# Kernel optimization log

Hardware: AMD Instinct MI355X
Metric: run time of the kernel (lower is better)

## Reference

```python
import math
import jax, jax.numpy as jnp
import numpy as np


def setup_inputs() -> dict:
    key = jax.random.key(0)
    ks = jax.random.split(key, 6)
    b, k, t, h = 4, 128, 2048, 8
    s = 0.05
    return {
        "x": jax.random.normal(ks[0], (b, k, t), dtype=jnp.float32),
        "Wq": jax.random.normal(ks[1], (h * k, k), dtype=jnp.float32) * s,
        "Wk": jax.random.normal(ks[2], (h * k, k), dtype=jnp.float32) * s,
        "Wv": jax.random.normal(ks[3], (h * k, k), dtype=jnp.float32) * s,
        "Wu": jax.random.normal(ks[4], (k, h * k), dtype=jnp.float32) * s,
        "bu": jax.random.normal(ks[5], (k,), dtype=jnp.float32) * s,
    }


def reference(x, Wq, Wk, Wv, Wu, bu):
    b, k, t = x.shape
    h = Wq.shape[0] // k

    def proj(W):
        # x: [b,k,t], W: [h*k, k] -> [b,h,k,t]
        return jnp.einsum('bkt,jk->bjt', x, W).reshape(b, h, k, t)

    q = proj(Wq)
    keys = proj(Wk)
    v = proj(Wv)

    # scores: [b,h,t,t], scaled by 1/sqrt(k)
    dot = jnp.einsum('bhkt,bhki->bhti', q, keys) / math.sqrt(k)
    attn = jax.nn.softmax(dot, axis=-1)

    # attend: [b,h,k,t]
    o = jnp.einsum('bhti,bhki->bhkt', attn, v)

    # unify heads: Wu [k, h*k] viewed as [k,h,k]
    Wu3 = Wu.reshape(k, h, k)
    out = jnp.einsum('bhet,khe->bkt', o, Wu3)
    return out + bu[None, :, None]
```

## Files before the change

kernel.cpp:

```cpp
#include <hip/hip_runtime.h>
#include <hip/hip_bf16.h>

using short8 = __attribute__((ext_vector_type(8))) short;
using f32x4  = __attribute__((ext_vector_type(4))) float;
using f32x16 = __attribute__((ext_vector_type(16))) float;
using uint2v = __attribute__((ext_vector_type(2))) unsigned;

#define B_  4
#define KD  128
#define T_  2048
#define H_  8
#define HK  (H_*KD)
#define NT  (T_/64)
#define VROW 72

__device__ __forceinline__ ushort f2bf(float f) {
    unsigned u = __builtin_bit_cast(unsigned, f);
    u += 0x7fffu + ((u >> 16) & 1u);
    return (ushort)(u >> 16);
}

__device__ __forceinline__ unsigned cvt_pk_bf16(float lo, float hi) {
    unsigned r;
    asm("v_cvt_pk_bf16_f32 %0, %1, %2" : "=v"(r) : "v"(lo), "v"(hi));
    return r;
}

__device__ __forceinline__ unsigned cvt_pk_fp8_lo(unsigned old, float a, float b) {
    unsigned r = old;
    asm("v_cvt_pk_fp8_f32 %0, %1, %2" : "+v"(r) : "v"(a), "v"(b));
    return r;
}
__device__ __forceinline__ unsigned cvt_pk_fp8_hi(unsigned old, float a, float b) {
    unsigned r = old;
    asm("v_cvt_pk_fp8_f32 %0, %1, %2 op_sel:[0,0,1]" : "+v"(r) : "v"(a), "v"(b));
    return r;
}

__global__ __launch_bounds__(256) void prep_kernel(const float* __restrict__ x,
                                                   const float* __restrict__ Wq,
                                                   const float* __restrict__ Wk,
                                                   const float* __restrict__ Wv,
                                                   const float* __restrict__ Wu,
                                                   ushort* __restrict__ wdst,
                                                   ushort* __restrict__ xt) {
    __shared__ float tile[64][65];
    int bx = blockIdx.x;
    if (bx < 2048) {
        int i = bx * 256 + threadIdx.x;
        const int n1 = HK * KD;
        const float* src = (i < n1) ? Wq : (i < 2*n1) ? Wk : (i < 3*n1) ? Wv : Wu;
        wdst[i] = f2bf(src[i & (n1 - 1)]);
        return;
    }
    int bi = bx - 2048;
    int t0 = (bi & 31) * 64;
    int k0 = ((bi >> 5) & 1) * 64;
    int b  = bi >> 6;
    int c  = threadIdx.x & 63;
    int r4 = threadIdx.x >> 6;
    #pragma unroll
    for (int i = 0; i < 16; i++) {
        int k = r4 * 16 + i;
        tile[k][c] = x[((size_t)b * KD + k0 + k) * T_ + t0 + c];
    }
    __syncthreads();
    #pragma unroll
    for (int i = 0; i < 16; i++) {
        int t = r4 * 16 + i;
        xt[((size_t)b * T_ + t0 + t) * KD + k0 + c] = f2bf(tile[c][t]);
    }
}

__global__ __launch_bounds__(256, 2) void proj_kernel(const ushort* __restrict__ xt,
                                                      const ushort* __restrict__ wall,
                                                      ushort* __restrict__ qtb,
                                                      ushort* __restrict__ ktb,
                                                      unsigned char* __restrict__ vsb) {
    int bz = blockIdx.y;
    int which = bz >> 2, b = bz & 3;
    int tidb = blockIdx.x;
    const ushort *A, *Bp;
    void* Cv;
    int N, m0, n0;
    float scale = 1.f;
    if (which < 2) {
        m0 = (tidb >> 3) * 128;
        n0 = (tidb & 7) * 128;
        A  = xt + (size_t)b * T_ * KD;
        Bp = wall + (size_t)which * (HK * KD);
        Cv = (which ? ktb : qtb) + (size_t)b * T_ * HK;
        N  = HK;
        if (which == 0) scale = 0.08838834764831845f;
    } else {
        m0 = (tidb >> 4) * 128;
        n0 = (tidb & 15) * 128;
        A  = wall + (size_t)2 * (HK * KD);
        Bp = xt + (size_t)b * T_ * KD;
        Cv = vsb + (size_t)b * HK * T_;
        N  = T_;
    }
    int lane = threadIdx.x & 63;
    int w    = threadIdx.x >> 6;
    int lq = lane & 31, hi = lane >> 5, hi8 = hi * 8;
    m0 += (w >> 1) * 64;
    n0 += (w & 1) * 64;

    const ushort* a0p = A  + (size_t)(m0 + lq) * KD + hi8;
    const ushort* a1p = A  + (size_t)(m0 + 32 + lq) * KD + hi8;
    const ushort* b0p = Bp + (size_t)(n0 + lq) * KD + hi8;
    const ushort* b1p = Bp + (size_t)(n0 + 32 + lq) * KD + hi8;

    short8 a0[8], a1[8], b0[8], b1[8];
    #pragma unroll
    for (int kc = 0; kc < 8; kc++) {
        a0[kc] = *(const short8*)(a0p + kc * 16);
        a1[kc] = *(const short8*)(a1p + kc * 16);
        b0[kc] = *(const short8*)(b0p + kc * 16);
        b1[kc] = *(const short8*)(b1p + kc * 16);
    }
    f32x16 acc[2][2] = {};
    #pragma unroll
    for (int kc = 0; kc < 8; kc++) {
        acc[0][0] = __builtin_amdgcn_mfma_f32_32x32x16_bf16(a0[kc], b0[kc], acc[0][0], 0, 0, 0);
        acc[0][1] = __builtin_amdgcn_mfma_f32_32x32x16_bf16(a0[kc], b1[kc], acc[0][1], 0, 0, 0);
        acc[1][0] = __builtin_amdgcn_mfma_f32_32x32x16_bf16(a1[kc], b0[kc], acc[1][0], 0, 0, 0);
        acc[1][1] = __builtin_amdgcn_mfma_f32_32x32x16_bf16(a1[kc], b1[kc], acc[1][1], 0, 0, 0);
    }
    if (which < 2) {
        ushort* C = (ushort*)Cv;
        #pragma unroll
        for (int i = 0; i < 2; i++)
            #pragma unroll
            for (int j = 0; j < 2; j++)
                #pragma unroll
                for (int r = 0; r < 16; r++) {
                    int m = m0 + i*32 + (r & 3) + 8 * (r >> 2) + 4 * hi;
                    int n = n0 + j*32 + lq;
                    C[(size_t)m * N + n] = f2bf(acc[i][j][r] * scale);
                }
    } else {
        unsigned char* C = (unsigned char*)Cv;
        #pragma unroll
        for (int i = 0; i < 2; i++)
            #pragma unroll
            for (int j = 0; j < 2; j++)
                #pragma unroll
                for (int r = 0; r < 16; r++) {
                    int m = m0 + i*32 + (r & 3) + 8 * (r >> 2) + 4 * hi;
                    int n = n0 + j*32 + lq;
                    float v = acc[i][j][r];
                    C[(size_t)m * N + n] = (unsigned char)(cvt_pk_fp8_lo(0u, v, v) & 0xffu);
                }
    }
}

__global__ __launch_bounds__(256) void gemm_abT_f32bias(const ushort* __restrict__ A,
                                                        const ushort* __restrict__ B, long sB,
                                                        const float* __restrict__ bias,
                                                        float* __restrict__ C, long sC,
                                                        int M, int N, int Kd) {
    int b = blockIdx.z;
    B += (long)b * sB;  C += (long)b * sC;
    int lane = threadIdx.x & 63;
    int w    = threadIdx.x >> 6;
    int lr = lane & 15, lg = lane >> 4;
    int m0 = blockIdx.x * 64 + (w >> 1) * 32;
    int n0 = blockIdx.y * 64 + (w & 1) * 32;

    f32x4 acc[2][2] = {};
    #pragma unroll 4
    for (int k0 = 0; k0 < Kd; k0 += 32) {
        short8 af[2], bf[2];
        #pragma unroll
        for (int i = 0; i < 2; i++)
            af[i] = *(const short8*)(A + (long)(m0 + i*16 + lr) * Kd + k0 + lg*8);
        #pragma unroll
        for (int j = 0; j < 2; j++)
            bf[j] = *(const short8*)(B + (long)(n0 + j*16 + lr) * Kd + k0 + lg*8);
        #pragma unroll
        for (int i = 0; i < 2; i++)
            #pragma unroll
            for (int j = 0; j < 2; j++)
                acc[i][j] = __builtin_amdgcn_mfma_f32_16x16x32_bf16(af[i], bf[j], acc[i][j], 0, 0, 0);
    }
    #pragma unroll
    for (int i = 0; i < 2; i++)
        #pragma unroll
        for (int j = 0; j < 2; j++)
            #pragma unroll
            for (int r = 0; r < 4; r++) {
                int m = m0 + i*16 + lg*4 + r;
                int n = n0 + j*16 + lr;
                C[(long)m * N + n] = acc[i][j][r] + bias[m];
            }
}

__global__ __launch_bounds__(512, 2) void attn32_kernel(const ushort* __restrict__ qt,
                                                        const ushort* __restrict__ kt,
                                                        const unsigned char* __restrict__ vs,
                                                        ushort* __restrict__ ot) {
    int f = blockIdx.x;
    int xcd = f & 7, u = f >> 3;
    int qt8 = u & 7, gh = u >> 3;
    int g = xcd + 8 * gh;
    int h = g & 7, b = g >> 3;
    int w    = threadIdx.x >> 6;
    int lane = threadIdx.x & 63;
    int lq = lane & 31, hi = lane >> 5;
    int hi8 = hi * 8;
    int q0w = qt8 * 256 + w * 32;

    __shared__ __align__(16) ushort k_lds[2][64 * 128];
    __shared__ __align__(16) unsigned char v_lds[2][128 * VROW];

    int tid  = threadIdx.x;
    int krow = tid >> 3, kcol = (tid & 7) << 4;
    const ushort* kst = kt + ((size_t)b * T_ + krow) * HK + h * KD + kcol;
    int kwi = krow * 128 + (kcol ^ ((krow & 7) << 3));
    int vrow = tid >> 2, vc16 = (tid & 3) << 4;
    const unsigned char* vst = vs + ((size_t)b * HK + h * KD + vrow) * T_ + vc16;
    int vwb = vrow * VROW + ((((vc16 >> 4) ^ (vrow & 3))) << 4);

    const ushort* qbase = qt + ((size_t)b * T_ + q0w + lq) * HK + h * KD + hi8;

    short8 qf[8];
    #pragma unroll
    for (int dc = 0; dc < 8; dc++)
        qf[dc] = *(const short8*)(qbase + dc * 16);

    short8 rk0 = *(const short8*)(kst);
    short8 rk1 = *(const short8*)(kst + 8);
    long rvlo = *(const long*)(vst);
    long rvhi = *(const long*)(vst + 8);
    *(short8*)&k_lds[0][kwi]     = rk0;
    *(short8*)&k_lds[0][kwi ^ 8] = rk1;
    *(long*)&v_lds[0][vwb]       = rvlo;
    *(long*)&v_lds[0][vwb + 8]   = rvhi;
    rk0 = *(const short8*)(kst + (size_t)64 * HK);
    rk1 = *(const short8*)(kst + (size_t)64 * HK + 8);
    rvlo = *(const long*)(vst + 64);
    rvhi = *(const long*)(vst + 64 + 8);
    __syncthreads();

    f32x16 o_acc[4] = {};
    float m_q = -1e30f, l_q = 0.f;
    const int xsw = (lq & 7) << 3;
    const int vsw = lq & 3;

    for (int t = 0; t < NT; ++t) {
        const int cur = t & 1;
        f32x16 s0 = {}, s1 = {};
        const ushort* kr0 = &k_lds[cur][(size_t)lq * 128];
        const ushort* kr1 = &k_lds[cur][(size_t)(32 + lq) * 128];
        #pragma unroll
        for (int dc = 0; dc < 8; dc++) {
            int c = (dc * 16 + hi8) ^ xsw;
            short8 kf0 = *(const short8*)(kr0 + c);
            short8 kf1 = *(const short8*)(kr1 + c);
            s0 = __builtin_amdgcn_mfma_f32_32x32x16_bf16(kf0, qf[dc], s0, 0, 0, 0);
            s1 = __builtin_amdgcn_mfma_f32_32x32x16_bf16(kf1, qf[dc], s1, 0, 0, 0);
        }

        float mx[8];
        #pragma unroll
        for (int i = 0; i < 8; i++)
            mx[i] = fmaxf(fmaxf(s0[i], s0[i+8]), fmaxf(s1[i], s1[i+8]));
        #pragma unroll
        for (int st = 4; st > 0; st >>= 1)
            #pragma unroll
            for (int i = 0; i < st; i++) mx[i] = fmaxf(mx[i], mx[i+st]);
        float pmax = fmaxf(mx[0], __shfl_xor(mx[0], 32));

        if (!__all(pmax - m_q <= 5.f)) {
            float mnew = fmaxf(m_q, pmax);
            float corr = __expf(m_q - mnew);
            l_q *= corr;
            m_q = mnew;
            #pragma unroll
            for (int r = 0; r < 16; r++) {
                float cr = __shfl(corr, (r & 3) + 8 * (r >> 2) + 4 * hi);
                #pragma unroll
                for (int dn = 0; dn < 4; dn++) o_acc[dn][r] *= cr;
            }
        }

        float ls0 = 0.f, ls1 = 0.f, ls2 = 0.f, ls3 = 0.f;
        #pragma unroll
        for (int r = 0; r < 16; r++) {
            float e0 = __expf(s0[r] - m_q);
            float e1 = __expf(s1[r] - m_q);
            s0[r] = e0; s1[r] = e1;
            if (r & 1) { ls1 += e0; ls3 += e1; } else { ls0 += e0; ls2 += e1; }
        }
        float lsum = (ls0 + ls1) + (ls2 + ls3);
        lsum += __shfl_xor(lsum, 32);
        l_q += lsum;

        long ap8[4];
        #pragma unroll
        for (int ks = 0; ks < 4; ks++) {
            const f32x16& sN = (ks < 2) ? s0 : s1;
            int rb = (ks & 1) * 8;
            unsigned F0 = cvt_pk_fp8_lo(0u, sN[rb+0], sN[rb+1]);
            F0 = cvt_pk_fp8_hi(F0, sN[rb+2], sN[rb+3]);
            unsigned F1 = cvt_pk_fp8_lo(0u, sN[rb+4], sN[rb+5]);
            F1 = cvt_pk_fp8_hi(F1, sN[rb+6], sN[rb+7]);
            uint2v d01 = __builtin_amdgcn_permlane32_swap(F0, F1, false, false);
            ap8[ks] = (long)(((unsigned long)d01[1] << 32) | (unsigned long)d01[0]);
        }

        #pragma unroll
        for (int dn = 0; dn < 4; dn++) {
            const unsigned char* vr = &v_lds[cur][(size_t)(dn*32 + lq) * VROW];
            #pragma unroll
            for (int ks = 0; ks < 4; ks++) {
                long vf = *(const long*)(vr + ((ks ^ vsw) << 4) + hi8);
                o_acc[dn] = __builtin_amdgcn_mfma_f32_32x32x16_fp8_fp8(ap8[ks], vf, o_acc[dn], 0, 0, 0);
            }
        }

        __syncthreads();
        if (t + 1 < NT) {
            const int nxt = cur ^ 1;
            *(short8*)&k_lds[nxt][kwi]     = rk0;
            *(short8*)&k_lds[nxt][kwi ^ 8] = rk1;
            *(long*)&v_lds[nxt][vwb]       = rvlo;
            *(long*)&v_lds[nxt][vwb + 8]   = rvhi;
            if (t + 2 < NT) {
                size_t ko = (size_t)(t + 2) * 64 * HK;
                int    vo = (t + 2) * 64;
                rk0 = *(const short8*)(kst + ko);
                rk1 = *(const short8*)(kst + ko + 8);
                rvlo = *(const long*)(vst + vo);
                rvhi = *(const long*)(vst + vo + 8);
            }
            __syncthreads();
        }
    }

    float linv = 1.f / l_q;
    ushort* ob = ot + ((size_t)b * T_ + q0w) * HK + h * KD;
    #pragma unroll
    for (int r = 0; r < 16; r++) {
        int qrow = (r & 3) + 8 * (r >> 2) + 4 * hi;
        float lr_ = __shfl(linv, qrow);
        #pragma unroll
        for (int dn = 0; dn < 4; dn++)
            ob[(size_t)qrow * HK + dn*32 + lq] = f2bf(o_acc[dn][r] * lr_);
    }
}

extern "C" void kernel_launch(void* const* d_in, const int* in_sizes, int n_in,
                              void* d_out, int out_size, void* d_ws, size_t ws_size,
                              hipStream_t stream) {
    const float* x  = (const float*)d_in[0];
    const float* Wq = (const float*)d_in[1];
    const float* Wk = (const float*)d_in[2];
    const float* Wv = (const float*)d_in[3];
    const float* Wu = (const float*)d_in[4];
    const float* bu = (const float*)d_in[5];
    float* out = (float*)d_out;

    const size_t XT  = (size_t)B_ * T_ * KD * 2;
    const size_t WB  = (size_t)HK * KD * 2;
    const size_t BIG = (size_t)B_ * T_ * HK * 2;
    const size_t VSZ = (size_t)B_ * HK * T_;
    size_t need = XT + 4*WB + 3*BIG + VSZ;
    if (ws_size < need) return;

    char* p = (char*)d_ws;
    ushort* xt  = (ushort*)p;            p += XT;
    ushort* wqb = (ushort*)p;            p += WB;
    ushort* wkb = (ushort*)p;            p += WB;
    ushort* wvb = (ushort*)p;            p += WB;
    ushort* wub = (ushort*)p;            p += WB;
    ushort* qtb = (ushort*)p;            p += BIG;
    ushort* ktb = (ushort*)p;            p += BIG;
    unsigned char* vsb = (unsigned char*)p;  p += VSZ;
    ushort* otb = (ushort*)p;            p += BIG;
    (void)wkb; (void)wvb;

    prep_kernel<<<2304, 256, 0, stream>>>(x, Wq, Wk, Wv, Wu, wqb, xt);

    proj_kernel<<<dim3(128, 12), 256, 0, stream>>>(xt, wqb, qtb, ktb, vsb);

    attn32_kernel<<<dim3(256), 512, 0, stream>>>(qtb, ktb, vsb, otb);

    gemm_abT_f32bias<<<dim3(KD/64, T_/64, B_), 256, 0, stream>>>(
        wub, otb, (long)T_*HK, bu, out, (long)KD*T_, KD, T_, HK);
}
```

Before: 122.8 us.

## Read K directly from global in attention and vectorize projection stores

The attention kernel no longer stages K tiles through double-buffered LDS. Each wave loads its K fragments straight from global memory (L2-cached) inside the loop, which frees LDS and removes the K store/swizzle work. The cost is redundant global K reads across the 8 waves and exposed load latency with no prefetch. The projection kernel also swaps its output tiling so each lane writes packed bf16x4 or fp8x4 words instead of scalar strided stores.

```diff
diff --git a/kernel.cpp b/kernel.cpp
--- a/kernel.cpp
+++ b/kernel.cpp
@@ -18,12 +18,6 @@
     unsigned u = __builtin_bit_cast(unsigned, f);
     u += 0x7fffu + ((u >> 16) & 1u);
     return (ushort)(u >> 16);
-}
-
-__device__ __forceinline__ unsigned cvt_pk_bf16(float lo, float hi) {
-    unsigned r;
-    asm("v_cvt_pk_bf16_f32 %0, %1, %2" : "=v"(r) : "v"(lo), "v"(hi));
-    return r;
 }
 
 __device__ __forceinline__ unsigned cvt_pk_fp8_lo(unsigned old, float a, float b) {
@@ -80,36 +74,34 @@
     int bz = blockIdx.y;
     int which = bz >> 2, b = bz & 3;
     int tidb = blockIdx.x;
-    const ushort *A, *Bp;
-    void* Cv;
-    int N, m0, n0;
-    float scale = 1.f;
-    if (which < 2) {
-        m0 = (tidb >> 3) * 128;
-        n0 = (tidb & 7) * 128;
-        A  = xt + (size_t)b * T_ * KD;
-        Bp = wall + (size_t)which * (HK * KD);
-        Cv = (which ? ktb : qtb) + (size_t)b * T_ * HK;
-        N  = HK;
-        if (which == 0) scale = 0.08838834764831845f;
-    } else {
-        m0 = (tidb >> 4) * 128;
-        n0 = (tidb & 15) * 128;
-        A  = wall + (size_t)2 * (HK * KD);
-        Bp = xt + (size_t)b * T_ * KD;
-        Cv = vsb + (size_t)b * HK * T_;
-        N  = T_;
-    }
     int lane = threadIdx.x & 63;
     int w    = threadIdx.x >> 6;
     int lq = lane & 31, hi = lane >> 5, hi8 = hi * 8;
-    m0 += (w >> 1) * 64;
-    n0 += (w & 1) * 64;
-
-    const ushort* a0p = A  + (size_t)(m0 + lq) * KD + hi8;
-    const ushort* a1p = A  + (size_t)(m0 + 32 + lq) * KD + hi8;
-    const ushort* b0p = Bp + (size_t)(n0 + lq) * KD + hi8;
-    const ushort* b1p = Bp + (size_t)(n0 + 32 + lq) * KD + hi8;
+
+    int tt0 = (tidb >> 3) * 128;
+    int jj0 = (tidb & 7) * 128;
+
+    const ushort *a0p, *a1p, *b0p, *b1p;
+    int m0, n0;
+    if (which < 2) {
+        m0 = jj0 + (w >> 1) * 64;
+        n0 = tt0 + (w & 1) * 64;
+        const ushort* A  = wall + (size_t)which * (HK * KD);
+        const ushort* Bp = xt + (size_t)b * T_ * KD;
+        a0p = A  + (size_t)(m0 + lq) * KD + hi8;
+        a1p = A  + (size_t)(m0 + 32 + lq) * KD + hi8;
+        b0p = Bp + (size_t)(n0 + lq) * KD + hi8;
+        b1p = Bp + (size_t)(n0 + 32 + lq) * KD + hi8;
+    } else {
+        m0 = tt0 + (w >> 1) * 64;
+        n0 = jj0 + (w & 1) * 64;
+        const ushort* A  = xt + (size_t)b * T_ * KD;
+        const ushort* Bp = wall + (size_t)2 * (HK * KD);
+        a0p = A  + (size_t)(m0 + lq) * KD + hi8;
+        a1p = A  + (size_t)(m0 + 32 + lq) * KD + hi8;
+        b0p = Bp + (size_t)(n0 + lq) * KD + hi8;
+        b1p = Bp + (size_t)(n0 + 32 + lq) * KD + hi8;
+    }
 
     short8 a0[8], a1[8], b0[8], b1[8];
     #pragma unroll
@@ -127,31 +119,43 @@
         acc[1][0] = __builtin_amdgcn_mfma_f32_32x32x16_bf16(a1[kc], b0[kc], acc[1][0], 0, 0, 0);
         acc[1][1] = __builtin_amdgcn_mfma_f32_32x32x16_bf16(a1[kc], b1[kc], acc[1][1], 0, 0, 0);
     }
+
     if (which < 2) {
-        ushort* C = (ushort*)Cv;
+        float scale = which ? 1.f : 0.08838834764831845f;
+        ushort* C = (which ? ktb : qtb) + (size_t)b * T_ * HK;
         #pragma unroll
         for (int i = 0; i < 2; i++)
             #pragma unroll
-            for (int j = 0; j < 2; j++)
+            for (int jj = 0; jj < 2; jj++) {
+                int t = n0 + jj*32 + lq;
                 #pragma unroll
-                for (int r = 0; r < 16; r++) {
-                    int m = m0 + i*32 + (r & 3) + 8 * (r >> 2) + 4 * hi;
-                    int n = n0 + j*32 + lq;
-                    C[(size_t)m * N + n] = f2bf(acc[i][j][r] * scale);
+                for (int qd = 0; qd < 4; qd++) {
+                    int jb = m0 + i*32 + 8*qd + 4*hi;
+                    const f32x16& a = acc[i][jj];
+                    unsigned u0 = (unsigned)f2bf(a[4*qd+0]*scale)
+                                | ((unsigned)f2bf(a[4*qd+1]*scale) << 16);
+                    unsigned u1 = (unsigned)f2bf(a[4*qd+2]*scale)
+                                | ((unsigned)f2bf(a[4*qd+3]*scale) << 16);
+                    uint2v uv; uv[0] = u0; uv[1] = u1;
+                    *(uint2v*)(C + (size_t)t * HK + jb) = uv;
                 }
+            }
     } else {
-        unsigned char* C = (unsigned char*)Cv;
+        unsigned char* C = vsb + (size_t)b * HK * T_;
         #pragma unroll
         for (int i = 0; i < 2; i++)
             #pragma unroll
-            for (int j = 0; j < 2; j++)
+            for (int jj = 0; jj < 2; jj++) {
+                int j = n0 + jj*32 + lq;
                 #pragma unroll
-                for (int r = 0; r < 16; r++) {
-                    int m = m0 + i*32 + (r & 3) + 8 * (r >> 2) + 4 * hi;
-                    int n = n0 + j*32 + lq;
-                    float v = acc[i][j][r];
-                    C[(size_t)m * N + n] = (unsigned char)(cvt_pk_fp8_lo(0u, v, v) & 0xffu);
+                for (int qd = 0; qd < 4; qd++) {
+                    int tb = m0 + i*32 + 8*qd + 4*hi;
+                    const f32x16& a = acc[i][jj];
+                    unsigned dw = cvt_pk_fp8_lo(0u, a[4*qd+0], a[4*qd+1]);
+                    dw = cvt_pk_fp8_hi(dw, a[4*qd+2], a[4*qd+3]);
+                    *(unsigned*)(C + (size_t)j * T_ + tb) = dw;
                 }
+            }
     }
 }
 
@@ -211,53 +215,43 @@
     int hi8 = hi * 8;
     int q0w = qt8 * 256 + w * 32;
 
-    __shared__ __align__(16) ushort k_lds[2][64 * 128];
     __shared__ __align__(16) unsigned char v_lds[2][128 * VROW];
 
     int tid  = threadIdx.x;
-    int krow = tid >> 3, kcol = (tid & 7) << 4;
-    const ushort* kst = kt + ((size_t)b * T_ + krow) * HK + h * KD + kcol;
-    int kwi = krow * 128 + (kcol ^ ((krow & 7) << 3));
     int vrow = tid >> 2, vc16 = (tid & 3) << 4;
     const unsigned char* vst = vs + ((size_t)b * HK + h * KD + vrow) * T_ + vc16;
     int vwb = vrow * VROW + ((((vc16 >> 4) ^ (vrow & 3))) << 4);
 
     const ushort* qbase = qt + ((size_t)b * T_ + q0w + lq) * HK + h * KD + hi8;
+    const ushort* kbase = kt + (size_t)b * T_ * HK + h * KD + hi8;
 
     short8 qf[8];
     #pragma unroll
     for (int dc = 0; dc < 8; dc++)
         qf[dc] = *(const short8*)(qbase + dc * 16);
 
-    short8 rk0 = *(const short8*)(kst);
-    short8 rk1 = *(const short8*)(kst + 8);
     long rvlo = *(const long*)(vst);
     long rvhi = *(const long*)(vst + 8);
-    *(short8*)&k_lds[0][kwi]     = rk0;
-    *(short8*)&k_lds[0][kwi ^ 8] = rk1;
     *(long*)&v_lds[0][vwb]       = rvlo;
     *(long*)&v_lds[0][vwb + 8]   = rvhi;
-    rk0 = *(const short8*)(kst + (size_t)64 * HK);
-    rk1 = *(const short8*)(kst + (size_t)64 * HK + 8);
     rvlo = *(const long*)(vst + 64);
     rvhi = *(const long*)(vst + 64 + 8);
     __syncthreads();
 
     f32x16 o_acc[4] = {};
     float m_q = -1e30f, l_q = 0.f;
-    const int xsw = (lq & 7) << 3;
     const int vsw = lq & 3;
 
     for (int t = 0; t < NT; ++t) {
         const int cur = t & 1;
+        const int kb = t * 64;
         f32x16 s0 = {}, s1 = {};
-        const ushort* kr0 = &k_lds[cur][(size_t)lq * 128];
-        const ushort* kr1 = &k_lds[cur][(size_t)(32 + lq) * 128];
+        const ushort* kp0 = kbase + (size_t)(kb + lq) * HK;
+        const ushort* kp1 = kbase + (size_t)(kb + 32 + lq) * HK;
         #pragma unroll
         for (int dc = 0; dc < 8; dc++) {
-            int c = (dc * 16 + hi8) ^ xsw;
-            short8 kf0 = *(const short8*)(kr0 + c);
-            short8 kf1 = *(const short8*)(kr1 + c);
+            short8 kf0 = *(const short8*)(kp0 + dc * 16);
+            short8 kf1 = *(const short8*)(kp1 + dc * 16);
             s0 = __builtin_amdgcn_mfma_f32_32x32x16_bf16(kf0, qf[dc], s0, 0, 0, 0);
             s1 = __builtin_amdgcn_mfma_f32_32x32x16_bf16(kf1, qf[dc], s1, 0, 0, 0);
         }
@@ -323,15 +317,10 @@
         __syncthreads();
         if (t + 1 < NT) {
             const int nxt = cur ^ 1;
-            *(short8*)&k_lds[nxt][kwi]     = rk0;
-            *(short8*)&k_lds[nxt][kwi ^ 8] = rk1;
             *(long*)&v_lds[nxt][vwb]       = rvlo;
             *(long*)&v_lds[nxt][vwb + 8]   = rvhi;
             if (t + 2 < NT) {
-                size_t ko = (size_t)(t + 2) * 64 * HK;
-                int    vo = (t + 2) * 64;
-                rk0 = *(const short8*)(kst + ko);
-                rk1 = *(const short8*)(kst + ko + 8);
+                int vo = (t + 2) * 64;
                 rvlo = *(const long*)(vst + vo);
                 rvhi = *(const long*)(vst + vo + 8);
             }
```

Result: slower. 228.9 us (+86.3%).
